# Optimization experiments

Hardware: AMD Instinct MI355X
Metric: run time of the kernel (lower is better)

The kernel has to match this reference:

```python
import jax, jax.numpy as jnp
import numpy as np

B, C, H, W = 16, 512, 32, 32
HW = H * W  # == input_features == output_features for shapes to be consistent


def setup_inputs() -> dict:
    key = jax.random.key(0)
    k1, k2, k3 = jax.random.split(key, 3)
    node1 = jax.random.normal(k1, (B, C, H, W), dtype=jnp.float32)
    node2 = jax.random.normal(k2, (B, C, H, W), dtype=jnp.float32)
    # nn.Linear(input_features, output_features, bias=False).weight: [out, in]
    W_c = jax.random.normal(k3, (HW, HW), dtype=jnp.float32) * (1.0 / np.sqrt(HW))
    return {"node1": node1, "node2": node2, "W_c": W_c}


def reference(node1, node2, W_c):
    b, c, h, w = node1.shape
    hw = h * w
    n1 = node1.reshape(b, c, hw)  # [B, C, HW]
    n2 = node2.reshape(b, c, hw)  # [B, C, HW]
    # x = W_c(n1): Linear applies y = x @ W^T  -> [B, C, HW_out]
    x = jnp.einsum('bch,oh->bco', n1, W_c)
    # e = bmm(x.permute(0,2,1), n2): [B, HW_out, C] @ [B, C, HW] -> [B, HW_out, HW]
    e = jnp.einsum('bco,bch->boh', x, n2)
    a = jax.nn.softmax(e, axis=-1)  # softmax over last dim (HW of node2)
    # m = bmm(n2, a): [B, C, HW] @ [B, HW, HW] -> [B, C, HW]
    m = jnp.einsum('bck,bkj->bcj', n2, a)
    return m
```

## Files before the change

kernel.cpp:

```cpp
#include <hip/hip_runtime.h>
#include <math.h>


typedef _Float16 f16;
typedef _Float16 f16x8 __attribute__((ext_vector_type(8)));
typedef _Float16 f16x4 __attribute__((ext_vector_type(4)));
typedef float f32x4 __attribute__((ext_vector_type(4)));

#define L2E 1.442695040888963f

#define WG_BARRIER() asm volatile("s_waitcnt lgkmcnt(0)\ns_barrier" ::: "memory")

__global__ __launch_bounds__(256) void prep(const float* __restrict__ n1,
                                            const float* __restrict__ Wc,
                                            const float* __restrict__ n2,
                                            f16* __restrict__ n1f, f16* __restrict__ Wf,
                                            f16* __restrict__ n2f, f16* __restrict__ n2t) {
    const int bid = blockIdx.x, tid = threadIdx.x;
    if (bid < 4608) {
        const float* s = (bid < 4096) ? n1 : Wc;
        f16* d = (bid < 4096) ? n1f : Wf;
        const size_t i = ((size_t)(bid < 4096 ? bid : bid - 4096) * 256 + tid) * 8;
        f32x4 a = *(const f32x4*)(s + i);
        f32x4 b = *(const f32x4*)(s + i + 4);
        f16x8 o;
        o[0] = (f16)a[0]; o[1] = (f16)a[1]; o[2] = (f16)a[2]; o[3] = (f16)a[3];
        o[4] = (f16)b[0]; o[5] = (f16)b[1]; o[6] = (f16)b[2]; o[7] = (f16)b[3];
        *(f16x8*)(d + i) = o;
        return;
    }
    const int id = bid - 4608;
    const int b = id >> 7;
    const int ry = (id & 127) >> 4;
    const int cx = id & 15;
    const float* S = n2 + (size_t)b * 512 * 1024;
    f16* Dn = n2f + (size_t)b * 512 * 1024;
    f16* Dt = n2t + (size_t)b * 1024 * 512;
    __shared__ f16 Ts[64 * 72];
    const int r0 = ry * 64, c0 = cx * 64;
    const int rr = tid >> 3, cc8 = (tid & 7) * 8;
#pragma unroll
    for (int h = 0; h < 2; ++h) {
        const int row = r0 + rr + 32 * h;
        const float* s = S + (size_t)row * 1024 + c0 + cc8;
        f32x4 a = *(const f32x4*)s, bq = *(const f32x4*)(s + 4);
        f16x8 o;
        o[0] = (f16)a[0]; o[1] = (f16)a[1]; o[2] = (f16)a[2]; o[3] = (f16)a[3];
        o[4] = (f16)bq[0]; o[5] = (f16)bq[1]; o[6] = (f16)bq[2]; o[7] = (f16)bq[3];
        *(f16x8*)&Ts[(rr + 32 * h) * 72 + cc8] = o;
        *(f16x8*)(Dn + (size_t)row * 1024 + c0 + cc8) = o;
    }
    __syncthreads();
    const int j = tid >> 2, k16 = (tid & 3) * 16;
    f16* d = Dt + (size_t)(c0 + j) * 512 + r0 + k16;
    f16x8 o0, o1;
#pragma unroll
    for (int i = 0; i < 8; ++i) {
        o0[i] = Ts[(k16 + i) * 72 + j];
        o1[i] = Ts[(k16 + 8 + i) * 72 + j];
    }
    *(f16x8*)d = o0;
    *(f16x8*)(d + 8) = o1;
}

__global__ __launch_bounds__(256) void stats_combine(const float* __restrict__ Pm,
                                                     const float* __restrict__ Ps,
                                                     float* __restrict__ Sc) {
    const int g = blockIdx.x * 256 + threadIdx.x;
    const int b = g >> 10, o = g & 1023;
    const int mt = o >> 8, ml = o & 255;
    const float* pm = Pm + ((size_t)(b * 4 + mt) * 16) * 256 + ml;
    const float* ps = Ps + ((size_t)(b * 4 + mt) * 16) * 256 + ml;
    float M = -3.0e38f;
#pragma unroll
    for (int p = 0; p < 16; ++p) M = fmaxf(M, pm[p * 256]);
    float S = 0.f;
#pragma unroll
    for (int p = 0; p < 16; ++p) S += ps[p * 256] * exp2f(pm[p * 256] - M);
    Sc[g] = M + __log2f(S);
}

__device__ __forceinline__ f16x8 expb(f16x8 b, f32x4 cl, f32x4 ch) {
    f16x8 t;
#pragma unroll
    for (int i = 0; i < 4; ++i) t[i] = (f16)exp2f(fmaf((float)b[i], L2E, -cl[i]));
#pragma unroll
    for (int i = 0; i < 4; ++i) t[4 + i] = (f16)exp2f(fmaf((float)b[4 + i], L2E, -ch[i]));
    return t;
}

template <int NS, bool EXPB>
__device__ __forceinline__ void gemm_core(const char* gA0, const char* gA1,
                                          const char* gB, const float* gSp,
                                          char* SM, int sOff, int wm, int wn,
                                          int col, int swz16, f32x4 (&acc)[4][4]) {
    f16x8 a00 = *(const f16x8*)gA0, a01 = *(const f16x8*)gA1;
    f16x8 b0 = *(const f16x8*)gB;
    f32x4 c00, c01, c10, c11;
    if (EXPB) { c00 = *(const f32x4*)gSp; c01 = *(const f32x4*)(gSp + 4); }
    {
        char* dA = SM + sOff;
        *(f16x8*)dA = a00;
        *(f16x8*)(dA + 8192) = a01;
        char* dB = SM + 32768 + sOff;
        *(f16x8*)dB = EXPB ? expb(b0, c00, c01) : b0;
    }
    f16x8 a10 = *(const f16x8*)(gA0 + 64), a11 = *(const f16x8*)(gA1 + 64);
    f16x8 b1 = *(const f16x8*)(gB + 64);
    if (EXPB) { c10 = *(const f32x4*)(gSp + 32); c11 = *(const f32x4*)(gSp + 36); }
    a00 = *(const f16x8*)(gA0 + 128); a01 = *(const f16x8*)(gA1 + 128);
    b0 = *(const f16x8*)(gB + 128);
    if (EXPB) { c00 = *(const f32x4*)(gSp + 64); c01 = *(const f32x4*)(gSp + 68); }
    WG_BARRIER();
#pragma unroll
    for (int kb = 0; kb < NS; ++kb) {
        const char* Ac = SM + (kb & 1) * 16384;
        const char* Bc = SM + 32768 + (kb & 1) * 8192;
        f16x8 fa[4], fb[4];
#pragma unroll
        for (int u = 0; u < 4; ++u)
            fa[u] = *(const f16x8*)(Ac + (wm + u * 16 + col) * 64 + swz16);
#pragma unroll
        for (int v = 0; v < 4; ++v)
            fb[v] = *(const f16x8*)(Bc + (wn + v * 16 + col) * 64 + swz16);
#pragma unroll
        for (int u = 0; u < 4; ++u)
#pragma unroll
            for (int v = 0; v < 4; ++v)
                acc[u][v] = __builtin_amdgcn_mfma_f32_16x16x32_f16(fa[u], fb[v],
                                                                   acc[u][v], 0, 0, 0);
        if (kb + 1 < NS) {
            char* dA = SM + ((kb + 1) & 1) * 16384 + sOff;
            char* dB = SM + 32768 + ((kb + 1) & 1) * 8192 + sOff;
            if ((kb & 1) == 0) {
                *(f16x8*)dA = a10;
                *(f16x8*)(dA + 8192) = a11;
                *(f16x8*)dB = EXPB ? expb(b1, c10, c11) : b1;
                if (kb + 3 < NS) {
                    a10 = *(const f16x8*)(gA0 + (size_t)(kb + 3) * 64);
                    a11 = *(const f16x8*)(gA1 + (size_t)(kb + 3) * 64);
                    b1 = *(const f16x8*)(gB + (size_t)(kb + 3) * 64);
                    if (EXPB) {
                        c10 = *(const f32x4*)(gSp + (size_t)(kb + 3) * 32);
                        c11 = *(const f32x4*)(gSp + (size_t)(kb + 3) * 32 + 4);
                    }
                }
            } else {
                *(f16x8*)dA = a00;
                *(f16x8*)(dA + 8192) = a01;
                *(f16x8*)dB = EXPB ? expb(b0, c00, c01) : b0;
                if (kb + 3 < NS) {
                    a00 = *(const f16x8*)(gA0 + (size_t)(kb + 3) * 64);
                    a01 = *(const f16x8*)(gA1 + (size_t)(kb + 3) * 64);
                    b0 = *(const f16x8*)(gB + (size_t)(kb + 3) * 64);
                    if (EXPB) {
                        c00 = *(const f32x4*)(gSp + (size_t)(kb + 3) * 32);
                        c01 = *(const f32x4*)(gSp + (size_t)(kb + 3) * 32 + 4);
                    }
                }
            }
            WG_BARRIER();
        }
    }
}

__device__ __forceinline__ void epilogue_tr(f32x4 (&acc)[4][4], char* SM, f16* dst0,
                                            int dstRow, int m0, int n0, int tid) {
    const int lane = tid & 63, wave = tid >> 6;
    const int col = lane & 15, quad = lane >> 4;
    const int wn = (wave >> 2) * 64;
    const int mh_w = (wave >> 1) & 1;
    const int wm_loc = (wave & 1) * 64;
    const int j = tid >> 2, seg = (tid & 3) * 32;
    WG_BARRIER();
    f16* Tt = (f16*)SM;
#pragma unroll
    for (int mh = 0; mh < 2; ++mh) {
        if (mh_w == mh) {
#pragma unroll
            for (int u = 0; u < 4; ++u)
#pragma unroll
                for (int v = 0; v < 4; ++v) {
                    f16x4 p;
#pragma unroll
                    for (int r = 0; r < 4; ++r) p[r] = (f16)acc[u][v][r];
                    *(f16x4*)&Tt[(wn + v * 16 + col) * 136 + wm_loc + u * 16 + quad * 4] = p;
                }
        }
        WG_BARRIER();
        f16* dst = dst0 + (size_t)(n0 + j) * dstRow + m0 + mh * 128 + seg;
#pragma unroll
        for (int c8 = 0; c8 < 32; c8 += 8)
            *(f16x8*)(dst + c8) = *(const f16x8*)&Tt[j * 136 + seg + c8];
        if (mh == 0) WG_BARRIER();
    }
}

__global__ __launch_bounds__(512) void gemm1_nt_xt(const f16* __restrict__ A,
                                                   const f16* __restrict__ Bw,
                                                   f16* __restrict__ Xt) {
    const int K = 1024;
    const int id = blockIdx.x;
    const int xcd = id & 7, loc = id >> 3;
    const int b = xcd * 2 + (loc >> 4);
    const int m0 = ((loc >> 3) & 1) * 256;
    const int n0 = (loc & 7) * 128;
    A += (size_t)b * 512 * K;
    Xt += (size_t)b * 1024 * 512;
    __shared__ __attribute__((aligned(16))) char SM[49152];
    const int tid = threadIdx.x, lane = tid & 63, wave = tid >> 6;
    const int col = lane & 15, quad = lane >> 4;
    const int wm = (wave & 3) * 64, wn = (wave >> 2) * 64;
    const int srow = tid >> 2, sslot = tid & 3;
    const int sOff = srow * 64 + ((sslot ^ ((srow >> 1) & 3)) * 16);
    const int swz16 = (quad ^ ((col >> 1) & 3)) * 16;
    const char* gA0 = (const char*)A + (size_t)(m0 + srow) * K * 2 + sslot * 16;
    const char* gA1 = gA0 + (size_t)128 * K * 2;
    const char* gB = (const char*)Bw + (size_t)(n0 + srow) * K * 2 + sslot * 16;
    f32x4 acc[4][4] = {};
    gemm_core<32, false>(gA0, gA1, gB, nullptr, SM, sOff, wm, wn, col, swz16, acc);
    epilogue_tr(acc, SM, Xt, 512, m0, n0, tid);
}

__global__ __launch_bounds__(512) void gemm2_nt_et(const f16* __restrict__ A,
                                                   const f16* __restrict__ B,
                                                   f16* __restrict__ Et,
                                                   float* __restrict__ Pm,
                                                   float* __restrict__ Ps) {
    const int K = 512;
    const int id = blockIdx.x;
    const int xcd = id & 7, loc = id >> 3;
    const int b = xcd * 2 + (loc >> 5);
    const int m0 = ((loc >> 3) & 3) * 256;
    const int n0 = (loc & 7) * 128;
    A += (size_t)b * 1024 * K;
    B += (size_t)b * 1024 * K;
    Et += (size_t)b * 1024 * 1024;
    __shared__ __attribute__((aligned(16))) char SM[49152];
    const int tid = threadIdx.x, lane = tid & 63, wave = tid >> 6;
    const int col = lane & 15, quad = lane >> 4;
    const int wm = (wave & 3) * 64, wn = (wave >> 2) * 64;
    const int srow = tid >> 2, sslot = tid & 3;
    const int sOff = srow * 64 + ((sslot ^ ((srow >> 1) & 3)) * 16);
    const int swz16 = (quad ^ ((col >> 1) & 3)) * 16;
    const char* gA0 = (const char*)A + (size_t)(m0 + srow) * K * 2 + sslot * 16;
    const char* gA1 = gA0 + (size_t)128 * K * 2;
    const char* gB = (const char*)B + (size_t)(n0 + srow) * K * 2 + sslot * 16;
    f32x4 acc[4][4] = {};
    gemm_core<16, false>(gA0, gA1, gB, nullptr, SM, sOff, wm, wn, col, swz16, acc);

    {
        float pm[16], ps[16];
#pragma unroll
        for (int u = 0; u < 4; ++u)
#pragma unroll
            for (int r = 0; r < 4; ++r) {
                float w0 = (float)(f16)acc[u][0][r] * L2E;
                float w1 = (float)(f16)acc[u][1][r] * L2E;
                float w2 = (float)(f16)acc[u][2][r] * L2E;
                float w3 = (float)(f16)acc[u][3][r] * L2E;
                float m2 = fmaxf(fmaxf(w0, w1), fmaxf(w2, w3));
                float s = exp2f(w0 - m2) + exp2f(w1 - m2) +
                          exp2f(w2 - m2) + exp2f(w3 - m2);
                pm[u * 4 + r] = m2;
                ps[u * 4 + r] = s;
            }
#pragma unroll
        for (int d = 1; d < 16; d <<= 1)
#pragma unroll
            for (int i = 0; i < 16; ++i) {
                float om = __shfl_xor(pm[i], d, 64);
                float os = __shfl_xor(ps[i], d, 64);
                float nm = fmaxf(pm[i], om);
                ps[i] = ps[i] * exp2f(pm[i] - nm) + os * exp2f(om - nm);
                pm[i] = nm;
            }
        if (col == 0) {
            const int part = ((b * 4 + (m0 >> 8)) * 8 + (n0 >> 7)) * 2 + (wave >> 2);
            float* bm = Pm + (size_t)part * 256;
            float* bs = Ps + (size_t)part * 256;
            const int wmq = (wave & 3) * 64 + quad * 4;
#pragma unroll
            for (int i = 0; i < 16; ++i) {
                const int ml = wmq + (i >> 2) * 16 + (i & 3);
                bm[ml] = pm[i];
                bs[ml] = ps[i];
            }
        }
    }

    epilogue_tr(acc, SM, Et, 1024, m0, n0, tid);
}

__global__ __launch_bounds__(512) void gemm3_nt_out(const f16* __restrict__ A,
                                                    const f16* __restrict__ Et,
                                                    const float* __restrict__ Sc,
                                                    float* __restrict__ C) {
    const int K = 1024;
    const int id = blockIdx.x;
    const int xcd = id & 7, loc = id >> 3;
    const int b = xcd * 2 + (loc >> 4);
    const int m0 = ((loc >> 3) & 1) * 256;
    const int n0 = (loc & 7) * 128;
    A += (size_t)b * 512 * K;
    Et += (size_t)b * 1024 * K;
    Sc += (size_t)b * 1024;
    C += (size_t)b * 512 * 1024;
    __shared__ __attribute__((aligned(16))) char SM[49152];
    const int tid = threadIdx.x, lane = tid & 63, wave = tid >> 6;
    const int col = lane & 15, quad = lane >> 4;
    const int wm = (wave & 3) * 64, wn = (wave >> 2) * 64;
    const int srow = tid >> 2, sslot = tid & 3;
    const int sOff = srow * 64 + ((sslot ^ ((srow >> 1) & 3)) * 16);
    const int swz16 = (quad ^ ((col >> 1) & 3)) * 16;
    const char* gA0 = (const char*)A + (size_t)(m0 + srow) * K * 2 + sslot * 16;
    const char* gA1 = gA0 + (size_t)128 * K * 2;
    const char* gB = (const char*)Et + (size_t)(n0 + srow) * K * 2 + sslot * 16;
    const float* gSp = Sc + sslot * 8;
    f32x4 acc[4][4] = {};
    gemm_core<32, true>(gA0, gA1, gB, gSp, SM, sOff, wm, wn, col, swz16, acc);

#pragma unroll
    for (int u = 0; u < 4; ++u)
#pragma unroll
        for (int v = 0; v < 4; ++v)
#pragma unroll
            for (int r = 0; r < 4; ++r)
                C[(size_t)(m0 + wm + u * 16 + quad * 4 + r) * 1024 + n0 + wn + v * 16 + col] =
                    acc[u][v][r];
}

extern "C" void kernel_launch(void* const* d_in, const int* in_sizes, int n_in,
                              void* d_out, int out_size, void* d_ws, size_t ws_size,
                              hipStream_t stream) {
    const float* n1 = (const float*)d_in[0];
    const float* n2 = (const float*)d_in[1];
    const float* Wc = (const float*)d_in[2];
    float* out = (float*)d_out;
    char* ws = (char*)d_ws;

    f16* n2t = (f16*)(ws);
    f16* Xt  = (f16*)(ws + (16u << 20));
    f16* Wf  = (f16*)(ws + (32u << 20));
    f16* Et  = (f16*)(ws + (32u << 20));
    f16* n1f = (f16*)(ws + (64u << 20));
    f16* n2f = (f16*)(ws + (80u << 20));
    float* Pm = (float*)(ws + (64u << 20));
    float* Ps = (float*)(ws + (65u << 20));
    float* Sc = (float*)(ws + (66u << 20));

    prep<<<6656, dim3(256), 0, stream>>>(n1, Wc, n2, n1f, Wf, n2f, n2t);
    gemm1_nt_xt<<<256, dim3(512), 0, stream>>>(n1f, Wf, Xt);
    gemm2_nt_et<<<512, dim3(512), 0, stream>>>(Xt, n2t, Et, Pm, Ps);
    stats_combine<<<64, dim3(256), 0, stream>>>(Pm, Ps, Sc);
    gemm3_nt_out<<<256, dim3(512), 0, stream>>>(n2f, Et, Sc, out);
}
```

Before: 216.5 us.

## Fuse softmax partial stats into transposed epilogue via shared-memory tile

Replaces the register-based per-wave softmax partial max/sum with 16-lane shuffle reductions and a separate transposed epilogue. The GEMM2 kernel now stages the tile transposed in shared memory in two halves, writes Et from it, and computes the row max/sum by scanning the staged tile. The result is one partial per 128-wide block instead of two per wave group, so the combine kernel reads 8 partials instead of 16. This aims to cut shuffle and exp work and the partial-stat traffic, at the cost of more LDS reads and extra barriers.

Result: faster. 202.7 us (-6.4%).

```diff
diff --git a/kernel.cpp b/kernel.cpp
--- a/kernel.cpp
+++ b/kernel.cpp
@@ -69,14 +69,14 @@
     const int g = blockIdx.x * 256 + threadIdx.x;
     const int b = g >> 10, o = g & 1023;
     const int mt = o >> 8, ml = o & 255;
-    const float* pm = Pm + ((size_t)(b * 4 + mt) * 16) * 256 + ml;
-    const float* ps = Ps + ((size_t)(b * 4 + mt) * 16) * 256 + ml;
+    const float* pm = Pm + ((size_t)(b * 4 + mt) * 8) * 256 + ml;
+    const float* ps = Ps + ((size_t)(b * 4 + mt) * 8) * 256 + ml;
     float M = -3.0e38f;
 #pragma unroll
-    for (int p = 0; p < 16; ++p) M = fmaxf(M, pm[p * 256]);
+    for (int p = 0; p < 8; ++p) M = fmaxf(M, pm[p * 256]);
     float S = 0.f;
 #pragma unroll
-    for (int p = 0; p < 16; ++p) S += ps[p * 256] * exp2f(pm[p * 256] - M);
+    for (int p = 0; p < 8; ++p) S += ps[p * 256] * exp2f(pm[p * 256] - M);
     Sc[g] = M + __log2f(S);
 }
 
@@ -250,46 +250,62 @@
     gemm_core<16, false>(gA0, gA1, gB, nullptr, SM, sOff, wm, wn, col, swz16, acc);
 
     {
-        float pm[16], ps[16];
-#pragma unroll
-        for (int u = 0; u < 4; ++u)
-#pragma unroll
-            for (int r = 0; r < 4; ++r) {
-                float w0 = (float)(f16)acc[u][0][r] * L2E;
-                float w1 = (float)(f16)acc[u][1][r] * L2E;
-                float w2 = (float)(f16)acc[u][2][r] * L2E;
-                float w3 = (float)(f16)acc[u][3][r] * L2E;
-                float m2 = fmaxf(fmaxf(w0, w1), fmaxf(w2, w3));
-                float s = exp2f(w0 - m2) + exp2f(w1 - m2) +
-                          exp2f(w2 - m2) + exp2f(w3 - m2);
-                pm[u * 4 + r] = m2;
-                ps[u * 4 + r] = s;
-            }
-#pragma unroll
-        for (int d = 1; d < 16; d <<= 1)
-#pragma unroll
-            for (int i = 0; i < 16; ++i) {
-                float om = __shfl_xor(pm[i], d, 64);
-                float os = __shfl_xor(ps[i], d, 64);
-                float nm = fmaxf(pm[i], om);
-                ps[i] = ps[i] * exp2f(pm[i] - nm) + os * exp2f(om - nm);
-                pm[i] = nm;
-            }
-        if (col == 0) {
-            const int part = ((b * 4 + (m0 >> 8)) * 8 + (n0 >> 7)) * 2 + (wave >> 2);
-            float* bm = Pm + (size_t)part * 256;
-            float* bs = Ps + (size_t)part * 256;
-            const int wmq = (wave & 3) * 64 + quad * 4;
-#pragma unroll
-            for (int i = 0; i < 16; ++i) {
-                const int ml = wmq + (i >> 2) * 16 + (i & 3);
-                bm[ml] = pm[i];
-                bs[ml] = ps[i];
-            }
+        const int wn_e = (wave >> 2) * 64;
+        const int mh_w = (wave >> 1) & 1;
+        const int wm_loc = (wave & 1) * 64;
+        const int j = tid >> 2, seg = (tid & 3) * 32;
+        const int scol = tid >> 2, srq = tid & 3;
+        WG_BARRIER();
+        f16* Tt = (f16*)SM;
+#pragma unroll
+        for (int mh = 0; mh < 2; ++mh) {
+            if (mh_w == mh) {
+#pragma unroll
+                for (int u = 0; u < 4; ++u)
+#pragma unroll
+                    for (int v = 0; v < 4; ++v) {
+                        f16x4 p;
+#pragma unroll
+                        for (int r = 0; r < 4; ++r) p[r] = (f16)acc[u][v][r];
+                        *(f16x4*)&Tt[(wn_e + v * 16 + col) * 136 + wm_loc + u * 16 + quad * 4] = p;
+                    }
+            }
+            WG_BARRIER();
+            f16* dst = Et + (size_t)(n0 + j) * 1024 + m0 + mh * 128 + seg;
+#pragma unroll
+            for (int c8 = 0; c8 < 32; c8 += 8)
+                *(f16x8*)(dst + c8) = *(const f16x8*)&Tt[j * 136 + seg + c8];
+            float mx = -3.0e38f;
+#pragma unroll
+            for (int n = 0; n < 32; ++n) {
+                const int row = srq * 32 + ((n + scol) & 31);
+                mx = fmaxf(mx, (float)Tt[row * 136 + scol]);
+            }
+            const float mxl = mx * L2E;
+            float s = 0.f;
+#pragma unroll
+            for (int n = 0; n < 32; ++n) {
+                const int row = srq * 32 + ((n + scol) & 31);
+                s += exp2f(fmaf((float)Tt[row * 136 + scol], L2E, -mxl));
+            }
+            float pmv = mxl, psv = s;
+#pragma unroll
+            for (int d = 1; d < 4; d <<= 1) {
+                float om = __shfl_xor(pmv, d, 64);
+                float os = __shfl_xor(psv, d, 64);
+                float nm = fmaxf(pmv, om);
+                psv = psv * exp2f(pmv - nm) + os * exp2f(om - nm);
+                pmv = nm;
+            }
+            if (srq == 0) {
+                const int part = (b * 4 + (m0 >> 8)) * 8 + (n0 >> 7);
+                const int ml = mh * 128 + scol;
+                Pm[(size_t)part * 256 + ml] = pmv;
+                Ps[(size_t)part * 256 + ml] = psv;
+            }
+            if (mh == 0) WG_BARRIER();
         }
     }
-
-    epilogue_tr(acc, SM, Et, 1024, m0, n0, tid);
 }
 
 __global__ __launch_bounds__(512) void gemm3_nt_out(const f16* __restrict__ A,
```
